# Performance work log

Hardware: AMD Instinct MI355X
Metric: run time of the kernel (lower is better)

The kernel has to match this reference:

```python
import jax, jax.numpy as jnp
import numpy as np

BLOCK = 16
H = 16
KV = 4
HPG = H // KV
DH = 64
SCALE = 1.0 / np.sqrt(DH).astype(np.float32)


def setup_inputs() -> dict:
    key = jax.random.key(0)
    ks = jax.random.split(key, 7)
    B, Ldec, Lenc, D = 2, 8192, 4096, 1024
    s = 1.0 / np.sqrt(D).astype(np.float32)
    return {
        "hidden_states": jax.random.normal(ks[0], (B, Ldec, D), jnp.float32),
        "encoder_hidden_states": jax.random.normal(ks[1], (B, Lenc, D), jnp.float32),
        "attention_mask": jax.random.randint(ks[2], (B, Lenc), 0, 2, jnp.int32),
        "Wq": jax.random.normal(ks[3], (D, H * DH), jnp.float32) * s,
        "Wk": jax.random.normal(ks[4], (D, KV * DH), jnp.float32) * s,
        "Wv": jax.random.normal(ks[5], (D, KV * DH), jnp.float32) * s,
        "Wo": jax.random.normal(ks[6], (H * DH, D), jnp.float32) * s,
    }


def reference(hidden_states, encoder_hidden_states, attention_mask, Wq, Wk, Wv, Wo):
    B, Ldec, D = hidden_states.shape
    Lenc = encoder_hidden_states.shape[1]
    pad = (BLOCK - Ldec % BLOCK) % BLOCK
    x = jnp.pad(hidden_states, ((0, 0), (0, pad), (0, 0))) if pad else hidden_states
    nb = (Ldec + pad) // BLOCK
    # mean-pool decoder tokens into blocks: [B, nb, D]
    pooled = x.reshape(B, nb, BLOCK, D).mean(axis=2)
    # projections; GQA: group q heads by kv head (repeat_interleave order)
    q = (pooled @ Wq).reshape(B, nb, KV, HPG, DH)          # [B, nb, KV, HPG, DH]
    k = (encoder_hidden_states @ Wk).reshape(B, Lenc, KV, DH)
    v = (encoder_hidden_states @ Wv).reshape(B, Lenc, KV, DH)
    scores = jnp.einsum("bngqd,blgd->bgqnl", q, k) * SCALE  # [B, KV, HPG, nb, Lenc]
    mask = (attention_mask == 0)[:, None, None, None, :]
    scores = jnp.where(mask, jnp.float32(-1e9), scores)
    attn = jax.nn.softmax(scores, axis=-1)
    out = jnp.einsum("bgqnl,blgd->bngqd", attn, v)          # [B, nb, KV, HPG, DH]
    out = out.reshape(B, nb, H * DH) @ Wo                   # [B, nb, D]
    # broadcast block output back to token level
    unpooled = jnp.broadcast_to(out[:, :, None, :], (B, nb, BLOCK, D)).reshape(B, nb * BLOCK, D)
    return unpooled[:, :Ldec, :]
```

## Files before the change

kernel.cpp:

```cpp
#include <hip/hip_runtime.h>


typedef unsigned short u16;
typedef __attribute__((ext_vector_type(8))) __bf16 bf16x8;
typedef __attribute__((ext_vector_type(4))) float f32x4;
typedef __attribute__((ext_vector_type(4))) _Float16 f16x4;

static __device__ __forceinline__ u16 f2bf(float f) {
    unsigned int u = __float_as_uint(f);
    u = (u + 0x7fffu + ((u >> 16) & 1u)) >> 16;
    return (u16)u;
}
static __device__ __forceinline__ void gload16(const u16* g, u16* l) {
    __builtin_amdgcn_global_load_lds(
        (const __attribute__((address_space(1))) void*)g,
        (__attribute__((address_space(3))) void*)l, 16, 0, 0);
}

__global__ __launch_bounds__(256) void prep_all(const float* __restrict__ enc,
                                                const float* __restrict__ hid,
                                                const int* __restrict__ mask,
                                                const float* __restrict__ Wq,
                                                const float* __restrict__ Wk,
                                                const float* __restrict__ Wv,
                                                const float* __restrict__ Wo,
                                                u16* __restrict__ encb,
                                                u16* __restrict__ poolb,
                                                u16* __restrict__ mh,
                                                u16* __restrict__ Wq_t,
                                                u16* __restrict__ Wkv_t,
                                                u16* __restrict__ Wo_t) {
    int bid = blockIdx.x;
    if (bid < 1024) {
        const int row = bid;
        const int c4 = threadIdx.x;
        const float4* src = (const float4*)(hid + (size_t)row * 16 * 1024) + c4;
        float4 v[16];
#pragma unroll
        for (int t = 0; t < 16; ++t) v[t] = src[(size_t)t * 256];
#pragma unroll
        for (int t = 0; t < 8; ++t) {
            v[t].x += v[t + 8].x; v[t].y += v[t + 8].y;
            v[t].z += v[t + 8].z; v[t].w += v[t + 8].w;
        }
#pragma unroll
        for (int t = 0; t < 4; ++t) {
            v[t].x += v[t + 4].x; v[t].y += v[t + 4].y;
            v[t].z += v[t + 4].z; v[t].w += v[t + 4].w;
        }
#pragma unroll
        for (int t = 0; t < 2; ++t) {
            v[t].x += v[t + 2].x; v[t].y += v[t + 2].y;
            v[t].z += v[t + 2].z; v[t].w += v[t + 2].w;
        }
        v[0].x += v[1].x; v[0].y += v[1].y; v[0].z += v[1].z; v[0].w += v[1].w;
        ushort4 o;
        o.x = f2bf(v[0].x * 0.0625f); o.y = f2bf(v[0].y * 0.0625f);
        o.z = f2bf(v[0].z * 0.0625f); o.w = f2bf(v[0].w * 0.0625f);
        *(ushort4*)(poolb + (size_t)row * 1024 + c4 * 4) = o;
    } else if (bid < 2048) {
        const int base = (bid - 1024) * 2048 + threadIdx.x;
        float4 v[8];
#pragma unroll
        for (int j = 0; j < 8; ++j) v[j] = ((const float4*)enc)[base + j * 256];
#pragma unroll
        for (int j = 0; j < 8; ++j) {
            ushort4 o;
            o.x = f2bf(v[j].x); o.y = f2bf(v[j].y);
            o.z = f2bf(v[j].z); o.w = f2bf(v[j].w);
            ((ushort4*)encb)[base + j * 256] = o;
        }
    } else if (bid < 4608) {
        bid -= 2048;
        const float* in; u16* out; int N, nbx, rowoff;
        if (bid < 1024)      { in = Wq; out = Wq_t;  N = 1024; nbx = 32; rowoff = 0; }
        else if (bid < 2048) { in = Wo; out = Wo_t;  N = 1024; nbx = 32; rowoff = 0; bid -= 1024; }
        else if (bid < 2304) { in = Wk; out = Wkv_t; N = 256;  nbx = 8;  rowoff = 0; bid -= 2048; }
        else                 { in = Wv; out = Wkv_t; N = 256;  nbx = 8;  rowoff = 256; bid -= 2304; }
        const int n0 = (bid % nbx) * 32, k0 = (bid / nbx) * 32;
        __shared__ float t[32][33];
        const int tx = threadIdx.x & 31, ty = threadIdx.x >> 5;
#pragma unroll
        for (int i = 0; i < 4; ++i)
            t[ty + 8 * i][tx] = in[(size_t)(k0 + ty + 8 * i) * N + n0 + tx];
        __syncthreads();
#pragma unroll
        for (int i = 0; i < 4; ++i)
            out[(size_t)(rowoff + n0 + ty + 8 * i) * 1024 + k0 + tx] = f2bf(t[tx][ty + 8 * i]);
    } else {
#pragma unroll
        for (int k = 0; k < 32; ++k) {
            const int i = threadIdx.x + 256 * k;
            mh[i] = mask[i] ? (u16)0x3C00 : (u16)0;
        }
    }
}

template <int MODE>
static __device__ __forceinline__ void gemm_core(const u16* __restrict__ A,
                                                 const u16* __restrict__ Bt,
                                                 u16* __restrict__ outQ,
                                                 float* __restrict__ out_f,
                                                 int m0, int n0, int kt0, int nkt,
                                                 u16* sAB) {
    u16* sA = sAB;
    u16* sB = sAB + 64 * 64;
    const int t = threadIdx.x;
    const int w = t >> 6, lane = t & 63, quad = lane >> 4, r16 = lane & 15;
    const int row8 = lane >> 3, seg = lane & 7;

    f32x4 acc[4];
#pragma unroll
    for (int i = 0; i < 4; ++i) acc[i] = (f32x4){0.f, 0.f, 0.f, 0.f};

    for (int kt = kt0; kt < kt0 + nkt; ++kt) {
        const int k0 = kt * 64;
        __syncthreads();
#pragma unroll
        for (int j = 0; j < 2; ++j) {
            const int ra = w * 16 + j * 8;
            gload16(A + (size_t)(m0 + ra + row8) * 1024 + k0 + seg * 8, sA + ra * 64);
            gload16(Bt + (size_t)(n0 + ra + row8) * 1024 + k0 + seg * 8, sB + ra * 64);
        }
        __syncthreads();
#pragma unroll
        for (int kk = 0; kk < 2; ++kk) {
            const bf16x8 af = *(const bf16x8*)(sA + (16 * w + r16) * 64 + kk * 32 + quad * 8);
#pragma unroll
            for (int nt = 0; nt < 4; ++nt) {
                const bf16x8 bfv = *(const bf16x8*)(sB + (nt * 16 + r16) * 64 + kk * 32 + quad * 8);
                acc[nt] = __builtin_amdgcn_mfma_f32_16x16x32_bf16(af, bfv, acc[nt], 0, 0, 0);
            }
        }
    }

    if (MODE == 0) {
#pragma unroll
        for (int nt = 0; nt < 4; ++nt)
#pragma unroll
            for (int r = 0; r < 4; ++r) {
                const int m = m0 + 16 * w + quad * 4 + r;
                const int c = n0 + nt * 16 + r16;
                const int b = m >> 9, nq = m & 511, g = c >> 8, qh = (c >> 6) & 3, d = c & 63;
                outQ[((((size_t)(b * 4 + g) * 4 + qh) * 512 + nq) << 6) + d] =
                    f2bf(acc[nt][r] * 0.180336880f);
            }
    } else {
#pragma unroll
        for (int nt = 0; nt < 4; ++nt)
#pragma unroll
            for (int r = 0; r < 4; ++r) {
                const int m = m0 + 16 * w + quad * 4 + r;
                const int c = n0 + nt * 16 + r16;
                out_f[(size_t)m * 1024 + c] = acc[nt][r];
            }
    }
}

__global__ __launch_bounds__(256) void gemm_qkv(const u16* __restrict__ poolb,
                                                const u16* __restrict__ encb,
                                                const u16* __restrict__ Wq_t,
                                                const u16* __restrict__ Wkv_t,
                                                const int* __restrict__ maskp,
                                                u16* __restrict__ Qa,
                                                u16* __restrict__ Ka,
                                                u16* __restrict__ Va) {
    __shared__ __align__(16) u16 smem[12288];
    const int bx = blockIdx.x;
    if (bx >= 512) {
        const int b = bx - 512;
        gemm_core<0>(poolb, Wq_t, Qa, nullptr, (b >> 4) * 64, (b & 15) * 64, 0, 16, smem);
        return;
    }
    const int m0 = (bx >> 3) * 128, n0 = (bx & 7) * 64;
    u16* sA = smem;
    u16* sB = smem + 128 * 64;
    const int t = threadIdx.x;
    const int w = t >> 6, lane = t & 63, quad = lane >> 4, r16 = lane & 15;
    const int row8 = lane >> 3, seg = lane & 7;

    f32x4 acc[2][4];
#pragma unroll
    for (int i = 0; i < 2; ++i)
#pragma unroll
        for (int nt = 0; nt < 4; ++nt) acc[i][nt] = (f32x4){0.f, 0.f, 0.f, 0.f};

    for (int kt = 0; kt < 16; ++kt) {
        const int k0 = kt * 64;
        __syncthreads();
#pragma unroll
        for (int p = 0; p < 4; ++p) {
            const int ra = p * 32 + w * 8;
            gload16(encb + (size_t)(m0 + ra + row8) * 1024 + k0 + seg * 8, sA + ra * 64);
        }
#pragma unroll
        for (int p = 0; p < 2; ++p) {
            const int ra = p * 32 + w * 8;
            gload16(Wkv_t + (size_t)(n0 + ra + row8) * 1024 + k0 + seg * 8, sB + ra * 64);
        }
        __syncthreads();
#pragma unroll
        for (int kk = 0; kk < 2; ++kk)
#pragma unroll
            for (int i = 0; i < 2; ++i) {
                const bf16x8 af = *(const bf16x8*)(sA + (w * 32 + i * 16 + r16) * 64 + kk * 32 + quad * 8);
#pragma unroll
                for (int nt = 0; nt < 4; ++nt) {
                    const bf16x8 bfv = *(const bf16x8*)(sB + (nt * 16 + r16) * 64 + kk * 32 + quad * 8);
                    acc[i][nt] = __builtin_amdgcn_mfma_f32_16x16x32_bf16(af, bfv, acc[i][nt], 0, 0, 0);
                }
            }
    }

    const bool isV = (n0 >= 256);
    const int g = (isV ? (n0 - 256) : n0) >> 6;
    const int b = m0 >> 12, l0 = m0 & 4095;
    __syncthreads();
    if (isV) {
        u16* sT = smem;
#pragma unroll
        for (int i = 0; i < 2; ++i) {
            float mfl[4];
#pragma unroll
            for (int r = 0; r < 4; ++r)
                mfl[r] = maskp[b * 4096 + l0 + w * 32 + i * 16 + quad * 4 + r] ? 1.f : 0.f;
#pragma unroll
            for (int nt = 0; nt < 4; ++nt)
#pragma unroll
                for (int r = 0; r < 4; ++r) {
                    const int ml = w * 32 + i * 16 + quad * 4 + r, cl = nt * 16 + r16;
                    union { _Float16 h; u16 u; } cv;
                    cv.h = (_Float16)(acc[i][nt][r] * mfl[r]);
                    sT[cl * 136 + ml] = cv.u;
                }
        }
        __syncthreads();
#pragma unroll
        for (int p = 0; p < 4; ++p) {
            const int idx = t + 256 * p, rr = idx >> 4, ch = idx & 15;
            *(int4*)(Va + ((size_t)(b * 4 + g) * 64 + rr) * 4096 + l0 + ch * 8) =
                *(const int4*)(sT + rr * 136 + ch * 8);
        }
    } else {
        u16* sT = smem;
#pragma unroll
        for (int i = 0; i < 2; ++i)
#pragma unroll
            for (int nt = 0; nt < 4; ++nt)
#pragma unroll
                for (int r = 0; r < 4; ++r) {
                    const int ml = w * 32 + i * 16 + quad * 4 + r, cl = nt * 16 + r16;
                    sT[ml * 72 + cl] = f2bf(acc[i][nt][r]);
                }
        __syncthreads();
#pragma unroll
        for (int p = 0; p < 4; ++p) {
            const int idx = t + 256 * p, rr = idx >> 3, ch = idx & 7;
            *(int4*)(Ka + (((size_t)(b * 4 + g) * 4096 + l0 + rr) << 6) + ch * 8) =
                *(const int4*)(sT + rr * 72 + ch * 8);
        }
    }
}

__global__ __launch_bounds__(256) void gemm_o_bcast(const u16* __restrict__ attn,
                                                    const u16* __restrict__ Wo_t,
                                                    float* __restrict__ out) {
    __shared__ __align__(16) u16 smem[2][8192];
    __shared__ __align__(16) float sf[64 * 68];
    const int bx = blockIdx.x;
    const int m0 = (bx >> 4) * 64, n0 = (bx & 15) * 64;
    const int t = threadIdx.x;
    const int w = t >> 6, lane = t & 63, quad = lane >> 4, r16 = lane & 15;
    const int row8 = lane >> 3, seg = lane & 7;

    f32x4 acc[4];
#pragma unroll
    for (int i = 0; i < 4; ++i) acc[i] = (f32x4){0.f, 0.f, 0.f, 0.f};

    auto stage = [&](int kt, int bi) {
        const int k0 = kt * 64;
        u16* sA = smem[bi];
        u16* sB = smem[bi] + 4096;
#pragma unroll
        for (int j = 0; j < 2; ++j) {
            const int ra = w * 16 + j * 8;
            gload16(attn + (size_t)(m0 + ra + row8) * 1024 + k0 + seg * 8, sA + ra * 64);
            gload16(Wo_t + (size_t)(n0 + ra + row8) * 1024 + k0 + seg * 8, sB + ra * 64);
        }
    };
    stage(0, 0);
    for (int kt = 0; kt < 16; ++kt) {
        const int bi = kt & 1;
        __syncthreads();
        if (kt < 15) stage(kt + 1, bi ^ 1);
        const u16* sA = smem[bi];
        const u16* sB = smem[bi] + 4096;
#pragma unroll
        for (int kk = 0; kk < 2; ++kk) {
            const bf16x8 af = *(const bf16x8*)(sA + (16 * w + r16) * 64 + kk * 32 + quad * 8);
#pragma unroll
            for (int nt = 0; nt < 4; ++nt) {
                const bf16x8 bfv = *(const bf16x8*)(sB + (nt * 16 + r16) * 64 + kk * 32 + quad * 8);
                acc[nt] = __builtin_amdgcn_mfma_f32_16x16x32_bf16(af, bfv, acc[nt], 0, 0, 0);
            }
        }
    }
    __syncthreads();
#pragma unroll
    for (int nt = 0; nt < 4; ++nt)
#pragma unroll
        for (int r = 0; r < 4; ++r)
            sf[(16 * w + quad * 4 + r) * 68 + nt * 16 + r16] = acc[nt][r];
    __syncthreads();
    const int rr = t >> 4, ch = t & 15;
#pragma unroll
    for (int i = 0; i < 4; ++i) {
        const int row = i * 16 + rr;
        const int m = m0 + row, b = m >> 9, n = m & 511;
        const float4 v = *(const float4*)(sf + row * 68 + ch * 4);
        float4* dst = (float4*)(out + ((size_t)b * 8192 + (size_t)n * 16) * 1024 + n0) + ch;
#pragma unroll
        for (int rep = 0; rep < 16; ++rep)
            dst[(size_t)rep * 256] = v;
    }
}

__global__ __launch_bounds__(256) void flash_attn(const u16* __restrict__ Qa,
                                                  const u16* __restrict__ Ka,
                                                  const u16* __restrict__ Vt,
                                                  const u16* __restrict__ mh,
                                                  u16* __restrict__ attnout) {
    const int bx = blockIdx.x;
    const int s16 = bx & 31, gb = bx >> 5;
    const int g = gb & 3, b = gb >> 2;
    __shared__ __align__(16) u16 sK[2][64 * 72];
    __shared__ __align__(16) u16 sV[2][64 * 68];
    const int t = threadIdx.x;
    const int qh = t >> 6, lane = t & 63, quad = lane >> 4, r16 = lane & 15;

    bf16x8 aq[2];
    {
        const size_t qbase = ((((size_t)(b * 4 + g) * 4 + qh) * 512) + s16 * 16 + r16) * 64;
#pragma unroll
        for (int kk = 0; kk < 2; ++kk)
            aq[kk] = *(const bf16x8*)(Qa + qbase + kk * 32 + quad * 8);
    }
    const u16* Kg = Ka + (size_t)(b * 4 + g) * 4096 * 64;
    const u16* Vg = Vt + (size_t)(b * 4 + g) * 64 * 4096;
    const u16* mb = mh + b * 4096 + quad * 4;

    const int row0 = t >> 3, seg0 = t & 7;
    const int row1 = (t + 256) >> 3, seg1 = t & 7;

    f32x4 o[4], lacc;
#pragma unroll
    for (int i = 0; i < 4; ++i) o[i] = (f32x4){0.f, 0.f, 0.f, 0.f};
    lacc = (f32x4){0.f, 0.f, 0.f, 0.f};

    int4 rk0, rk1, rv0, rv1;
    auto ldtile = [&](int l0) {
        rk0 = *(const int4*)(Kg + (size_t)(l0 + row0) * 64 + seg0 * 8);
        rk1 = *(const int4*)(Kg + (size_t)(l0 + row1) * 64 + seg1 * 8);
        rv0 = *(const int4*)(Vg + (size_t)row0 * 4096 + l0 + seg0 * 8);
        rv1 = *(const int4*)(Vg + (size_t)row1 * 4096 + l0 + seg1 * 8);
    };
    auto sttile = [&](int bi) {
        *(int4*)(sK[bi] + row0 * 72 + seg0 * 8) = rk0;
        *(int4*)(sK[bi] + row1 * 72 + seg1 * 8) = rk1;
        *(int4*)(sV[bi] + row0 * 68 + seg0 * 8) = rv0;
        *(int4*)(sV[bi] + row1 * 68 + seg1 * 8) = rv1;
    };

    ldtile(0);
    sttile(0);
    __syncthreads();

#pragma unroll 2
    for (int tile = 0; tile < 64; ++tile) {
        const int bi = tile & 1;
        const int l0 = tile * 64;
        if (tile < 63) ldtile(l0 + 64);

        f32x4 st[4];
#pragma unroll
        for (int nt = 0; nt < 4; ++nt) st[nt] = (f32x4){0.f, 0.f, 0.f, 0.f};
#pragma unroll
        for (int kk = 0; kk < 2; ++kk)
#pragma unroll
            for (int nt = 0; nt < 4; ++nt) {
                const bf16x8 ka = *(const bf16x8*)(sK[bi] + (nt * 16 + r16) * 72 + kk * 32 + quad * 8);
                st[nt] = __builtin_amdgcn_mfma_f32_16x16x32_bf16(ka, aq[kk], st[nt], 0, 0, 0);
            }

#pragma unroll
        for (int nt = 0; nt < 4; ++nt) {
            f16x4 pa;
#pragma unroll
            for (int j = 0; j < 4; ++j)
                pa[j] = (_Float16)__builtin_amdgcn_exp2f(st[nt][j]);
            const f16x4 bvm = *(const f16x4*)(mb + l0 + nt * 16);
            lacc = __builtin_amdgcn_mfma_f32_16x16x16f16(pa, bvm, lacc, 0, 0, 0);
#pragma unroll
            for (int dt = 0; dt < 4; ++dt) {
                const f16x4 bv = *(const f16x4*)(sV[bi] + (dt * 16 + r16) * 68 + nt * 16 + quad * 4);
                o[dt] = __builtin_amdgcn_mfma_f32_16x16x16f16(pa, bv, o[dt], 0, 0, 0);
            }
        }

        if (tile < 63) sttile(bi ^ 1);
        __syncthreads();
    }

    const size_t obase = ((size_t)b * 512 + s16 * 16) * 1024 + (g * 4 + qh) * 64;
#pragma unroll
    for (int r = 0; r < 4; ++r) {
        const float invL = 1.f / lacc[r];
        const size_t rbase = obase + (size_t)(quad * 4 + r) * 1024;
#pragma unroll
        for (int dt = 0; dt < 4; ++dt)
            attnout[rbase + dt * 16 + r16] = f2bf(o[dt][r] * invL);
    }
}

extern "C" void kernel_launch(void* const* d_in, const int* in_sizes, int n_in,
                              void* d_out, int out_size, void* d_ws, size_t ws_size,
                              hipStream_t stream) {
    const float* hid  = (const float*)d_in[0];
    const float* enc  = (const float*)d_in[1];
    const int*   mask = (const int*)d_in[2];
    const float* Wq   = (const float*)d_in[3];
    const float* Wk   = (const float*)d_in[4];
    const float* Wv   = (const float*)d_in[5];
    const float* Wo   = (const float*)d_in[6];
    float* out = (float*)d_out;

    char* ws = (char*)d_ws;
    size_t off = 0;
    auto alloc = [&](size_t bytes) -> char* {
        char* p = ws + off;
        off += (bytes + 255) & ~(size_t)255;
        return p;
    };
    u16* Wq_t  = (u16*)alloc((size_t)1024 * 1024 * 2);
    u16* Wkv_t = (u16*)alloc((size_t)512 * 1024 * 2);
    u16* Wo_t  = (u16*)alloc((size_t)1024 * 1024 * 2);
    u16* encb  = (u16*)alloc((size_t)8192 * 1024 * 2);
    u16* poolb = (u16*)alloc((size_t)1024 * 1024 * 2);
    u16* Qa    = (u16*)alloc((size_t)1024 * 1024 * 2);
    u16* Ka    = (u16*)alloc((size_t)8 * 4096 * 64 * 2);
    u16* Va    = (u16*)alloc((size_t)8 * 4096 * 64 * 2);
    u16* attn  = (u16*)alloc((size_t)1024 * 1024 * 2);
    u16* mh    = (u16*)alloc((size_t)8192 * 2);

    prep_all<<<4609, 256, 0, stream>>>(enc, hid, mask, Wq, Wk, Wv, Wo,
                                       encb, poolb, mh, Wq_t, Wkv_t, Wo_t);
    gemm_qkv<<<768, 256, 0, stream>>>(poolb, encb, Wq_t, Wkv_t, mask, Qa, Ka, Va);
    flash_attn<<<256, 256, 0, stream>>>(Qa, Ka, Va, mh, attn);
    gemm_o_bcast<<<256, 256, 0, stream>>>(attn, Wo_t, out);
}
```

Before: 261.4 us.

## Split flash attention KV range across four wave groups and swizzle LDS

The flash attention kernel now launches 1024 threads per block. Four wave groups each process an interleaved quarter of the KV tiles and their partial outputs and row sums are reduced through shared memory. The padded LDS layout is replaced by an XOR-swizzled layout, and both flash_attn and gemm_qkv block indices are remapped so neighbouring blocks land on the same XCD and share K/V or A tiles in cache. The aim is more waves per CU to hide latency, in exchange for a cross-group reduction step and losing the double-buffered prefetch into LDS.

```diff
diff --git a/kernel.cpp b/kernel.cpp
--- a/kernel.cpp
+++ b/kernel.cpp
@@ -172,7 +172,9 @@
         gemm_core<0>(poolb, Wq_t, Qa, nullptr, (b >> 4) * 64, (b & 15) * 64, 0, 16, smem);
         return;
     }
-    const int m0 = (bx >> 3) * 128, n0 = (bx & 7) * 64;
+    const int xcd = bx & 7, j = bx >> 3;
+    const int mt = xcd * 8 + (j & 7), nt2 = j >> 3;
+    const int m0 = mt * 128, n0 = nt2 * 64;
     u16* sA = smem;
     u16* sB = smem + 128 * 64;
     const int t = threadIdx.x;
@@ -325,32 +327,37 @@
     }
 }
 
-__global__ __launch_bounds__(256) void flash_attn(const u16* __restrict__ Qa,
-                                                  const u16* __restrict__ Ka,
-                                                  const u16* __restrict__ Vt,
-                                                  const u16* __restrict__ mh,
-                                                  u16* __restrict__ attnout) {
+__global__ __launch_bounds__(1024, 4) void flash_attn(const u16* __restrict__ Qa,
+                                                      const u16* __restrict__ Ka,
+                                                      const u16* __restrict__ Vt,
+                                                      const u16* __restrict__ mh,
+                                                      u16* __restrict__ attnout) {
     const int bx = blockIdx.x;
-    const int s16 = bx & 31, gb = bx >> 5;
+    const int gb = bx & 7, s16 = bx >> 3;
     const int g = gb & 3, b = gb >> 2;
-    __shared__ __align__(16) u16 sK[2][64 * 72];
-    __shared__ __align__(16) u16 sV[2][64 * 68];
+    __shared__ __align__(16) u16 sKV[4][2][4096];
     const int t = threadIdx.x;
-    const int qh = t >> 6, lane = t & 63, quad = lane >> 4, r16 = lane & 15;
+    const int wv = t >> 6, grp = wv >> 2, qh = wv & 3;
+    const int lane = t & 63, quad = lane >> 4, r16 = lane & 15;
+
+    u16* sK = sKV[grp][0];
+    u16* sV = sKV[grp][1];
 
     bf16x8 aq[2];
     {
-        const size_t qbase = ((((size_t)(b * 4 + g) * 4 + qh) * 512) + s16 * 16 + r16) * 64;
+        const size_t qbase = ((((size_t)gb * 4 + qh) * 512) + s16 * 16 + r16) * 64;
 #pragma unroll
         for (int kk = 0; kk < 2; ++kk)
             aq[kk] = *(const bf16x8*)(Qa + qbase + kk * 32 + quad * 8);
     }
-    const u16* Kg = Ka + (size_t)(b * 4 + g) * 4096 * 64;
-    const u16* Vg = Vt + (size_t)(b * 4 + g) * 64 * 4096;
+    const u16* Kg = Ka + (size_t)gb * 4096 * 64;
+    const u16* Vg = Vt + (size_t)gb * 64 * 4096;
     const u16* mb = mh + b * 4096 + quad * 4;
 
-    const int row0 = t >> 3, seg0 = t & 7;
-    const int row1 = (t + 256) >> 3, seg1 = t & 7;
+    const int tg = t & 255;
+    const int r0 = tg >> 3, ks = tg & 7, r1 = r0 + 32;
+    const int off0 = (r0 * 64 + ks * 8) ^ ((r0 & 7) << 3);
+    const int off1 = (r1 * 64 + ks * 8) ^ ((r1 & 7) << 3);
 
     f32x4 o[4], lacc;
 #pragma unroll
@@ -359,27 +366,24 @@
 
     int4 rk0, rk1, rv0, rv1;
     auto ldtile = [&](int l0) {
-        rk0 = *(const int4*)(Kg + (size_t)(l0 + row0) * 64 + seg0 * 8);
-        rk1 = *(const int4*)(Kg + (size_t)(l0 + row1) * 64 + seg1 * 8);
-        rv0 = *(const int4*)(Vg + (size_t)row0 * 4096 + l0 + seg0 * 8);
-        rv1 = *(const int4*)(Vg + (size_t)row1 * 4096 + l0 + seg1 * 8);
+        rk0 = *(const int4*)(Kg + (size_t)(l0 + r0) * 64 + ks * 8);
+        rk1 = *(const int4*)(Kg + (size_t)(l0 + r1) * 64 + ks * 8);
+        rv0 = *(const int4*)(Vg + (size_t)r0 * 4096 + l0 + ks * 8);
+        rv1 = *(const int4*)(Vg + (size_t)r1 * 4096 + l0 + ks * 8);
     };
-    auto sttile = [&](int bi) {
-        *(int4*)(sK[bi] + row0 * 72 + seg0 * 8) = rk0;
-        *(int4*)(sK[bi] + row1 * 72 + seg1 * 8) = rk1;
-        *(int4*)(sV[bi] + row0 * 68 + seg0 * 8) = rv0;
-        *(int4*)(sV[bi] + row1 * 68 + seg1 * 8) = rv1;
+    auto sttile = [&]() {
+        *(int4*)(sK + off0) = rk0;
+        *(int4*)(sK + off1) = rk1;
+        *(int4*)(sV + off0) = rv0;
+        *(int4*)(sV + off1) = rv1;
     };
 
-    ldtile(0);
-    sttile(0);
-    __syncthreads();
-
-#pragma unroll 2
-    for (int tile = 0; tile < 64; ++tile) {
-        const int bi = tile & 1;
-        const int l0 = tile * 64;
-        if (tile < 63) ldtile(l0 + 64);
+    ldtile(grp * 64);
+    for (int i = 0; i < 16; ++i) {
+        const int l0 = (i * 4 + grp) * 64;
+        sttile();
+        __syncthreads();
+        if (i < 15) ldtile(l0 + 256);
 
         f32x4 st[4];
 #pragma unroll
@@ -388,7 +392,8 @@
         for (int kk = 0; kk < 2; ++kk)
 #pragma unroll
             for (int nt = 0; nt < 4; ++nt) {
-                const bf16x8 ka = *(const bf16x8*)(sK[bi] + (nt * 16 + r16) * 72 + kk * 32 + quad * 8);
+                const int kidx = ((nt * 16 + r16) * 64 + kk * 32 + quad * 8) ^ ((r16 & 7) << 3);
+                const bf16x8 ka = *(const bf16x8*)(sK + kidx);
                 st[nt] = __builtin_amdgcn_mfma_f32_16x16x32_bf16(ka, aq[kk], st[nt], 0, 0, 0);
             }
 
@@ -402,23 +407,52 @@
             lacc = __builtin_amdgcn_mfma_f32_16x16x16f16(pa, bvm, lacc, 0, 0, 0);
 #pragma unroll
             for (int dt = 0; dt < 4; ++dt) {
-                const f16x4 bv = *(const f16x4*)(sV[bi] + (dt * 16 + r16) * 68 + nt * 16 + quad * 4);
+                const int vidx = ((dt * 16 + r16) * 64 + nt * 16 + quad * 4) ^ ((r16 & 7) << 3);
+                const f16x4 bv = *(const f16x4*)(sV + vidx);
                 o[dt] = __builtin_amdgcn_mfma_f32_16x16x16f16(pa, bv, o[dt], 0, 0, 0);
             }
         }
-
-        if (tile < 63) sttile(bi ^ 1);
-        __syncthreads();
-    }
-
-    const size_t obase = ((size_t)b * 512 + s16 * 16) * 1024 + (g * 4 + qh) * 64;
-#pragma unroll
-    for (int r = 0; r < 4; ++r) {
-        const float invL = 1.f / lacc[r];
-        const size_t rbase = obase + (size_t)(quad * 4 + r) * 1024;
+        __syncthreads();
+    }
+
+    float* fp = (float*)sKV;
+    if (grp > 0) {
 #pragma unroll
         for (int dt = 0; dt < 4; ++dt)
-            attnout[rbase + dt * 16 + r16] = f2bf(o[dt][r] * invL);
+#pragma unroll
+            for (int r = 0; r < 4; ++r)
+                fp[(grp - 1) * 4096 + qh * 1024 + (quad * 4 + r) * 64 + dt * 16 + r16] = o[dt][r];
+        if (r16 == 0) {
+#pragma unroll
+            for (int r = 0; r < 4; ++r)
+                fp[12288 + ((grp - 1) * 4 + qh) * 16 + quad * 4 + r] = lacc[r];
+        }
+    }
+    __syncthreads();
+    if (grp == 0) {
+        float Ls[4];
+#pragma unroll
+        for (int r = 0; r < 4; ++r) Ls[r] = lacc[r];
+#pragma unroll
+        for (int p = 0; p < 3; ++p) {
+#pragma unroll
+            for (int dt = 0; dt < 4; ++dt)
+#pragma unroll
+                for (int r = 0; r < 4; ++r)
+                    o[dt][r] += fp[p * 4096 + qh * 1024 + (quad * 4 + r) * 64 + dt * 16 + r16];
+#pragma unroll
+            for (int r = 0; r < 4; ++r)
+                Ls[r] += fp[12288 + (p * 4 + qh) * 16 + quad * 4 + r];
+        }
+        const size_t obase = ((size_t)b * 512 + s16 * 16) * 1024 + (g * 4 + qh) * 64;
+#pragma unroll
+        for (int r = 0; r < 4; ++r) {
+            const float invL = 1.f / Ls[r];
+            const size_t rbase = obase + (size_t)(quad * 4 + r) * 1024;
+#pragma unroll
+            for (int dt = 0; dt < 4; ++dt)
+                attnout[rbase + dt * 16 + r16] = f2bf(o[dt][r] * invL);
+        }
     }
 }
 
@@ -455,6 +489,6 @@
     prep_all<<<4609, 256, 0, stream>>>(enc, hid, mask, Wq, Wk, Wv, Wo,
                                        encb, poolb, mh, Wq_t, Wkv_t, Wo_t);
     gemm_qkv<<<768, 256, 0, stream>>>(poolb, encb, Wq_t, Wkv_t, mask, Qa, Ka, Va);
-    flash_attn<<<256, 256, 0, stream>>>(Qa, Ka, Va, mh, attn);
+    flash_attn<<<256, 1024, 0, stream>>>(Qa, Ka, Va, mh, attn);
     gemm_o_bcast<<<256, 256, 0, stream>>>(attn, Wo_t, out);
 }
```

Result: faster. 234.9 us (-10.1%).
